# Optimization experiments

Measured on AMD Instinct MI355X. Metric: run time of the kernel, lower is better.

The kernel has to match this reference:

```python
import jax, jax.numpy as jnp
import numpy as np

HID = 4096      # hidden_size
H = 32          # num_attention_heads
K = 8           # num_key_value_heads
D = HID // H    # head_dim = 128
G = H // K      # q heads per kv group = 4
INTER = 14336   # intermediate_size
T = 2048        # tokens (prefill)
EPS = 1e-5
THETA = 1000000.0


def setup_inputs() -> dict:
    key = jax.random.key(0)
    ks = jax.random.split(key, 9)
    s = 0.02
    return {
        "hidden_states": jax.random.normal(ks[0], (T, HID), jnp.float32),
        "position_ids": jnp.arange(T, dtype=jnp.int64),
        "wqkv": jax.random.normal(ks[1], ((H + 2 * K) * D, HID), jnp.float32) * s,
        "wo": jax.random.normal(ks[2], (HID, HID), jnp.float32) * s,
        "w1": jax.random.normal(ks[3], (INTER, HID), jnp.float32) * s,  # gate
        "w3": jax.random.normal(ks[4], (INTER, HID), jnp.float32) * s,  # up
        "w2": jax.random.normal(ks[5], (HID, INTER), jnp.float32) * s,  # down
        "attn_norm_w": jnp.ones((HID,), jnp.float32),
        "ffn_norm_w": jnp.ones((HID,), jnp.float32),
    }


def _rmsnorm(x, w):
    var = jnp.mean(jnp.square(x), axis=-1, keepdims=True)
    return x * jax.lax.rsqrt(var + EPS) * w


def _rope(x, cos, sin):
    # non-interleaved (half-split) rotation; x: [T, h, D], cos/sin: [T, 1, D//2]
    x1, x2 = x[..., : D // 2], x[..., D // 2 :]
    return jnp.concatenate([x1 * cos - x2 * sin, x2 * cos + x1 * sin], axis=-1)


def _attention(x, position_ids, wqkv, wo):
    t = x.shape[0]
    qkv = x @ wqkv.T  # [T, (H+2K)*D]
    q = qkv[:, : H * D].reshape(t, H, D)
    k = qkv[:, H * D : (H + K) * D].reshape(t, K, D)
    v = qkv[:, (H + K) * D :].reshape(t, K, D)

    inv_freq = 1.0 / (THETA ** (jnp.arange(0, D, 2, dtype=jnp.float32) / D))
    freqs = position_ids.astype(jnp.float32)[:, None] * inv_freq  # [T, D//2]
    cos = jnp.cos(freqs)[:, None, :]
    sin = jnp.sin(freqs)[:, None, :]
    q = _rope(q, cos, sin)
    k = _rope(k, cos, sin)

    # grouped-query attention: [T, K, G, D] queries vs [T, K, D] keys
    qg = q.reshape(t, K, G, D)
    scale = 1.0 / jnp.sqrt(jnp.float32(D))
    scores = jnp.einsum("tkgd,skd->kgts", qg, k) * scale  # [K, G, T, T]
    causal = jnp.tril(jnp.ones((t, t), dtype=bool))
    scores = jnp.where(causal, scores, jnp.finfo(scores.dtype).min)
    probs = jax.nn.softmax(scores, axis=-1)
    out = jnp.einsum("kgts,skd->tkgd", probs, v).reshape(t, H * D)
    return out @ wo.T


def _mlp(x, w1, w3, w2):
    return (jax.nn.silu(x @ w1.T) * (x @ w3.T)) @ w2.T


def reference(hidden_states, position_ids, wqkv, wo, w1, w3, w2, attn_norm_w, ffn_norm_w):
    h = hidden_states + _attention(_rmsnorm(hidden_states, attn_norm_w), position_ids, wqkv, wo)
    return h + _mlp(_rmsnorm(h, ffn_norm_w), w1, w3, w2)
```

## Files before the change

### kernel.cpp

```cpp
#include <hip/hip_runtime.h>
#include <stdint.h>

#define T_SEQ 2048
#define HIDN  4096
#define NH    32
#define NKV   8
#define DH    128
#define INTER 14336
#define QKV_N 6144
#define EPSR  1e-5f
#define SCALE 0.08838834764831845f
#define KVB   64

typedef __bf16 bf16x8 __attribute__((ext_vector_type(8)));
typedef float  f32x4  __attribute__((ext_vector_type(4)));

__device__ __forceinline__ f32x4 mfma16(bf16x8 a, bf16x8 b, f32x4 c) {
  return __builtin_amdgcn_mfma_f32_16x16x32_bf16(a, b, c, 0, 0, 0);
}

__device__ __forceinline__ void glds16(const void* g, void* l) {
  __builtin_amdgcn_global_load_lds(
      (__attribute__((address_space(1))) void*)g,
      (__attribute__((address_space(3))) void*)l,
      16, 0, 0);
}

__global__ __launch_bounds__(256) void cvt_bf16_kernel(
    const float* __restrict__ src, __bf16* __restrict__ dst, long n) {
  long stride = (long)gridDim.x * 256 * 8;
  for (long i = ((long)blockIdx.x * 256 + threadIdx.x) * 8; i < n; i += stride) {
    float4 a = *(const float4*)(src + i);
    float4 b = *(const float4*)(src + i + 4);
    bf16x8 o;
    o[0]=(__bf16)a.x; o[1]=(__bf16)a.y; o[2]=(__bf16)a.z; o[3]=(__bf16)a.w;
    o[4]=(__bf16)b.x; o[5]=(__bf16)b.y; o[6]=(__bf16)b.z; o[7]=(__bf16)b.w;
    *(bf16x8*)(dst + i) = o;
  }
}

__global__ __launch_bounds__(256) void rmsnorm_kernel(
    const float* __restrict__ x, const float* __restrict__ w,
    __bf16* __restrict__ y) {
  const int row = blockIdx.x, tid = threadIdx.x;
  const float* xr = x + (size_t)row * HIDN + tid * 16;
  float4 v0 = ((const float4*)xr)[0];
  float4 v1 = ((const float4*)xr)[1];
  float4 v2 = ((const float4*)xr)[2];
  float4 v3 = ((const float4*)xr)[3];
  float ss = v0.x*v0.x + v0.y*v0.y + v0.z*v0.z + v0.w*v0.w
           + v1.x*v1.x + v1.y*v1.y + v1.z*v1.z + v1.w*v1.w
           + v2.x*v2.x + v2.y*v2.y + v2.z*v2.z + v2.w*v2.w
           + v3.x*v3.x + v3.y*v3.y + v3.z*v3.z + v3.w*v3.w;
  #pragma unroll
  for (int off = 32; off >= 1; off >>= 1) ss += __shfl_xor(ss, off, 64);
  __shared__ float red[4];
  if ((tid & 63) == 0) red[tid >> 6] = ss;
  __syncthreads();
  float rn = rsqrtf((red[0] + red[1] + red[2] + red[3]) * (1.0f / HIDN) + EPSR);
  const float* wr = w + tid * 16;
  float4 w0 = ((const float4*)wr)[0];
  float4 w1v = ((const float4*)wr)[1];
  float4 w2v = ((const float4*)wr)[2];
  float4 w3v = ((const float4*)wr)[3];
  bf16x8 o0, o1;
  o0[0]=(__bf16)(v0.x*rn*w0.x);  o0[1]=(__bf16)(v0.y*rn*w0.y);
  o0[2]=(__bf16)(v0.z*rn*w0.z);  o0[3]=(__bf16)(v0.w*rn*w0.w);
  o0[4]=(__bf16)(v1.x*rn*w1v.x); o0[5]=(__bf16)(v1.y*rn*w1v.y);
  o0[6]=(__bf16)(v1.z*rn*w1v.z); o0[7]=(__bf16)(v1.w*rn*w1v.w);
  o1[0]=(__bf16)(v2.x*rn*w2v.x); o1[1]=(__bf16)(v2.y*rn*w2v.y);
  o1[2]=(__bf16)(v2.z*rn*w2v.z); o1[3]=(__bf16)(v2.w*rn*w2v.w);
  o1[4]=(__bf16)(v3.x*rn*w3v.x); o1[5]=(__bf16)(v3.y*rn*w3v.y);
  o1[6]=(__bf16)(v3.z*rn*w3v.z); o1[7]=(__bf16)(v3.w*rn*w3v.w);
  __bf16* yo = y + (size_t)row * HIDN + tid * 16;
  *(bf16x8*)(yo)     = o0;
  *(bf16x8*)(yo + 8) = o1;
}

template<int EPI>
__global__ __launch_bounds__(512, 2) void gemm256_kernel(
    const __bf16* __restrict__ A, const __bf16* __restrict__ B,
    void* __restrict__ Cout, int M, int N, int Kfull, int KZ) {
  extern __shared__ __align__(16) char smem[];
  const int tid = threadIdx.x;
  const int lane = tid & 63;
  const int wv = tid >> 6;
  const int wm = wv >> 2;
  const int wn = wv & 3;
  const int lr = lane & 15, ql = lane >> 4;

  const int gx = gridDim.x, gy = gridDim.y;
  const int nwg = gx * gy;
  const int orig = blockIdx.y * gx + blockIdx.x;
  const int cpx = nwg >> 3;
  const int swz = (orig & 7) * cpx + (orig >> 3);
  const int by = swz % gy, bx = swz / gy;
  const int m0 = by * 256, n0 = bx * 256;
  const int kbase = blockIdx.z * KZ;
  const int NT = KZ >> 6;

  const int u0 = tid, u1 = tid + 512;
  const int r0 = u0 >> 2, r1 = u1 >> 2;
  const int p0 = (u0 & 3) ^ ((r0 >> 1) & 3);
  const int p1 = (u1 & 3) ^ ((r1 >> 1) & 3);
  const char* aR0 = (const char*)(A + (size_t)(m0 + r0) * Kfull + kbase) + p0 * 16;
  const char* aR1 = (const char*)(A + (size_t)(m0 + r1) * Kfull + kbase) + p1 * 16;
  const char* bR0 = (const char*)(B + (size_t)(n0 + r0) * Kfull + kbase) + p0 * 16;
  const char* bR1 = (const char*)(B + (size_t)(n0 + r1) * Kfull + kbase) + p1 * 16;
  const int d0 = u0 * 16, d1 = u1 * 16;

  const int sA = ql ^ ((lr >> 1) & 3);
  int aoff[8], boff[4];
  #pragma unroll
  for (int mt = 0; mt < 8; mt++) aoff[mt] = (wm * 128 + mt * 16 + lr) * 64 + sA * 16;
  #pragma unroll
  for (int nt = 0; nt < 4; nt++) boff[nt] = (wn * 64 + nt * 16 + lr) * 64 + sA * 16;

#define STAGE_A(t, kh, b) do {                                         \
    const size_t _o = (size_t)(t) * 128 + (kh) * 64;                   \
    glds16(aR0 + _o, smem + (b) * 65536 + (kh) * 16384 + d0);          \
    glds16(aR1 + _o, smem + (b) * 65536 + (kh) * 16384 + d1);          \
  } while (0)
#define STAGE_B(t, kh, b) do {                                         \
    const size_t _o = (size_t)(t) * 128 + (kh) * 64;                   \
    glds16(bR0 + _o, smem + (b) * 65536 + 32768 + (kh) * 16384 + d0);  \
    glds16(bR1 + _o, smem + (b) * 65536 + 32768 + (kh) * 16384 + d1);  \
  } while (0)
#define LDA4(dst, mb, b, ks) do {                                      \
    const char* _p = smem + (b) * 65536 + (ks) * 16384;                \
    dst[0] = *(const bf16x8*)(_p + aoff[(mb) + 0]);                    \
    dst[1] = *(const bf16x8*)(_p + aoff[(mb) + 1]);                    \
    dst[2] = *(const bf16x8*)(_p + aoff[(mb) + 2]);                    \
    dst[3] = *(const bf16x8*)(_p + aoff[(mb) + 3]);                    \
  } while (0)
#define LDB4(b, ks) do {                                               \
    const char* _p = smem + (b) * 65536 + 32768 + (ks) * 16384;        \
    bfr[0] = *(const bf16x8*)(_p + boff[0]);                           \
    bfr[1] = *(const bf16x8*)(_p + boff[1]);                           \
    bfr[2] = *(const bf16x8*)(_p + boff[2]);                           \
    bfr[3] = *(const bf16x8*)(_p + boff[3]);                           \
  } while (0)
#define VMW8() asm volatile("s_waitcnt vmcnt(8)" ::: "memory")
#define BAR()  __builtin_amdgcn_s_barrier()
#define WAITK() do { asm volatile("s_waitcnt lgkmcnt(0)" ::: "memory"); \
    __builtin_amdgcn_sched_barrier(0); } while (0)
#define MFMA16(mb, AF) do {                                            \
    __builtin_amdgcn_s_setprio(1);                                     \
    _Pragma("unroll") for (int _m = 0; _m < 4; _m++)                   \
      _Pragma("unroll") for (int _n = 0; _n < 4; _n++)                 \
        acc[(mb) + _m][_n] = mfma16(AF[_m], bfr[_n], acc[(mb) + _m][_n]); \
    __builtin_amdgcn_s_setprio(0);                                     \
  } while (0)

  f32x4 acc[8][4] = {};
  bf16x8 afA[4], afB[4], bfr[4];

  STAGE_A(0, 0, 0); STAGE_B(0, 0, 0);
  STAGE_A(0, 1, 0); STAGE_B(0, 1, 0);
  STAGE_A(1, 0, 1); STAGE_B(1, 0, 1);
  VMW8();
  BAR();

  const int NI = NT >> 1;
  for (int i = 0; i < NI; ++i) {
    const int t1 = 2 * i + 1;
    const int s2 = (2 * i + 2 < NT) ? 2 * i + 2 : NT - 1;
    const int s3 = (2 * i + 3 < NT) ? 2 * i + 3 : NT - 1;
    LDA4(afA, 0, 0, 0); LDB4(0, 0);
    STAGE_A(t1, 1, 1);
    BAR(); WAITK(); MFMA16(0, afA); BAR();
    LDA4(afB, 4, 0, 0);
    STAGE_B(t1, 1, 1);
    VMW8(); BAR(); WAITK(); MFMA16(4, afB); BAR();
    LDA4(afA, 0, 0, 1); LDB4(0, 1);
    STAGE_A(s2, 0, 0);
    BAR(); WAITK(); MFMA16(0, afA); BAR();
    LDA4(afB, 4, 0, 1);
    STAGE_B(s2, 0, 0);
    VMW8(); BAR(); WAITK(); MFMA16(4, afB); BAR();
    LDA4(afA, 0, 1, 0); LDB4(1, 0);
    STAGE_A(s2, 1, 0);
    BAR(); WAITK(); MFMA16(0, afA); BAR();
    LDA4(afB, 4, 1, 0);
    STAGE_B(s2, 1, 0);
    VMW8(); BAR(); WAITK(); MFMA16(4, afB); BAR();
    LDA4(afA, 0, 1, 1); LDB4(1, 1);
    STAGE_A(s3, 0, 1);
    BAR(); WAITK(); MFMA16(0, afA); BAR();
    LDA4(afB, 4, 1, 1);
    STAGE_B(s3, 0, 1);
    VMW8(); BAR(); WAITK(); MFMA16(4, afB); BAR();
  }
  asm volatile("s_waitcnt vmcnt(0)" ::: "memory");

#undef STAGE_A
#undef STAGE_B
#undef LDA4
#undef LDB4
#undef VMW8
#undef BAR
#undef WAITK
#undef MFMA16

  #pragma unroll
  for (int mt = 0; mt < 8; mt++) {
    #pragma unroll
    for (int r = 0; r < 4; r++) {
      int rr = m0 + wm * 128 + mt * 16 + ql * 4 + r;
      #pragma unroll
      for (int nt = 0; nt < 4; nt++) {
        int cc = n0 + wn * 64 + nt * 16 + lr;
        size_t ix = (size_t)rr * N + cc;
        float val = acc[mt][nt][r];
        if (EPI == 0) ((float*)Cout)[(size_t)blockIdx.z * M * N + ix] = val;
        else          ((__bf16*)Cout)[ix] = (__bf16)val;
      }
    }
  }
}

__global__ __launch_bounds__(256) void add3_kernel(
    const float* __restrict__ p, const float* __restrict__ r,
    float* __restrict__ o, long n) {
  long stride = (long)gridDim.x * 1024;
  for (long i = ((long)blockIdx.x * 256 + threadIdx.x) * 4; i < n; i += stride) {
    float4 a = *(const float4*)(p + i);
    float4 b = *(const float4*)(p + n + i);
    float4 c = *(const float4*)(r + i);
    float4 o4;
    o4.x = a.x + b.x + c.x; o4.y = a.y + b.y + c.y;
    o4.z = a.z + b.z + c.z; o4.w = a.w + b.w + c.w;
    *(float4*)(o + i) = o4;
  }
}

__global__ __launch_bounds__(256) void rope_kernel(
    const __bf16* __restrict__ qkv, __bf16* __restrict__ q_r,
    __bf16* __restrict__ k_r) {
  const int t = blockIdx.x, tid = threadIdx.x;
  __shared__ float cs[64], sn[64];
  if (tid < 64) {
    float inv = exp2f(-(float)tid * (19.931568569324174f / 64.0f));
    float f = (float)t * inv;
    cs[tid] = cosf(f);
    sn[tid] = sinf(f);
  }
  __syncthreads();
  const __bf16* row = qkv + (size_t)t * QKV_N;
  for (int it = tid; it < 40 * 64; it += 256) {
    int hh = it >> 6, i = it & 63;
    float x1 = (float)row[hh * 128 + i];
    float x2 = (float)row[hh * 128 + 64 + i];
    float c = cs[i], s = sn[i];
    float o1 = x1 * c - x2 * s;
    float o2 = x2 * c + x1 * s;
    if (hh < NH) {
      __bf16* qo = q_r + (size_t)t * HIDN + hh * 128;
      qo[i] = (__bf16)o1;
      qo[64 + i] = (__bf16)o2;
    } else {
      __bf16* ko = k_r + (size_t)t * (NKV * DH) + (hh - NH) * 128;
      ko[i] = (__bf16)o1;
      ko[64 + i] = (__bf16)o2;
    }
  }
}

__global__ __launch_bounds__(256) void vtrans_kernel(
    const __bf16* __restrict__ qkv, __bf16* __restrict__ v_t) {
  __shared__ __bf16 tile[64][136];
  const int tid = threadIdx.x;
  const int t0 = blockIdx.x * 64, kh = blockIdx.y;
  #pragma unroll
  for (int i = 0; i < 4; i++) {
    int u = i * 256 + tid;
    int row = u >> 4, c = (u & 15) * 8;
    *(bf16x8*)&tile[row][c] =
        *(const bf16x8*)(qkv + (size_t)(t0 + row) * QKV_N + (NH + NKV) * DH + kh * DH + c);
  }
  __syncthreads();
  const int d = tid & 127, th = (tid >> 7) * 32;
  #pragma unroll
  for (int j = 0; j < 4; j++) {
    int t = th + j * 8;
    bf16x8 o;
    #pragma unroll
    for (int e = 0; e < 8; e++) o[e] = tile[t + e][d];
    *(bf16x8*)(v_t + ((size_t)kh * DH + d) * T_SEQ + t0 + t) = o;
  }
}

__global__ __launch_bounds__(256) void attn_kernel(
    const __bf16* __restrict__ q_r, const __bf16* __restrict__ k_r,
    const __bf16* __restrict__ v_t, __bf16* __restrict__ attn_o) {
  __shared__ __align__(16) __bf16 Ks[KVB * 128];
  __shared__ __align__(16) __bf16 Vs[128 * KVB];
  __shared__ __align__(16) __bf16 Pl[4 * 16 * KVB];

  const int tid = threadIdx.x;
  const int lane = tid & 63, wv = tid >> 6;
  const int lr = lane & 15, g = lane >> 4;
  const int qt = gridDim.x - 1 - blockIdx.x;
  const int h = blockIdx.y;
  const int kh = h >> 2;
  const int q0b = qt * 64;
  const int q0w = q0b + wv * 16;

  bf16x8 qf[4];
  {
    const __bf16* qp = q_r + (size_t)(q0w + lr) * HIDN + h * DH + g * 8;
    #pragma unroll
    for (int kk = 0; kk < 4; kk++) qf[kk] = *(const bf16x8*)(qp + kk * 32);
  }

  f32x4 o[8] = {};
  float mrun[4] = {-1e30f, -1e30f, -1e30f, -1e30f};
  float lrun[4] = {0.f, 0.f, 0.f, 0.f};
  char* PlW = (char*)Pl + wv * 2048;

  for (int kv0 = 0; kv0 < q0b + KVB; kv0 += KVB) {
    __syncthreads();
    #pragma unroll
    for (int i = 0; i < 4; i++) {
      int u = i * 256 + tid;
      int row = u >> 4;
      int cb = ((u & 15) * 16) ^ ((row & 7) << 4);
      glds16((const char*)(k_r + (size_t)(kv0 + row) * (NKV * DH) + kh * DH) + cb,
             (char*)Ks + u * 16);
    }
    #pragma unroll
    for (int i = 0; i < 4; i++) {
      int u = i * 256 + tid;
      int row = u >> 3;
      int cb = ((u & 7) * 16) ^ ((row & 7) << 4);
      glds16((const char*)(v_t + ((size_t)kh * DH + row) * T_SEQ + kv0) + cb,
             (char*)Vs + u * 16);
    }
    __syncthreads();

    if (q0w + 15 >= kv0) {
      f32x4 s[4] = {};
      #pragma unroll
      for (int kk = 0; kk < 4; kk++) {
        #pragma unroll
        for (int jt = 0; jt < 4; jt++) {
          int krow = jt * 16 + lr;
          int cb = (kk * 64 + g * 16) ^ ((krow & 7) << 4);
          bf16x8 kf = *(const bf16x8*)((char*)Ks + krow * 256 + cb);
          s[jt] = mfma16(qf[kk], kf, s[jt]);
        }
      }
      const bool need_mask = (kv0 + KVB - 1) > q0w;
      #pragma unroll
      for (int r = 0; r < 4; r++) {
        int qpos = q0w + g * 4 + r;
        int prow = g * 4 + r;
        float p[4];
        #pragma unroll
        for (int jt = 0; jt < 4; jt++) {
          float v = s[jt][r] * SCALE;
          if (need_mask && (kv0 + jt * 16 + lr > qpos)) v = -1e30f;
          p[jt] = v;
        }
        float mx = fmaxf(fmaxf(p[0], p[1]), fmaxf(p[2], p[3]));
        #pragma unroll
        for (int off = 1; off < 16; off <<= 1) mx = fmaxf(mx, __shfl_xor(mx, off, 64));
        float mn = fmaxf(mrun[r], mx);
        float corr = __expf(mrun[r] - mn);
        mrun[r] = mn;
        float ps = 0.f;
        #pragma unroll
        for (int jt = 0; jt < 4; jt++) {
          p[jt] = __expf(p[jt] - mn);
          ps += p[jt];
          int cbyte = ((jt * 16 + lr) * 2) ^ ((prow & 7) << 4);
          *(__bf16*)(PlW + prow * 128 + cbyte) = (__bf16)p[jt];
        }
        #pragma unroll
        for (int off = 1; off < 16; off <<= 1) ps += __shfl_xor(ps, off, 64);
        lrun[r] = lrun[r] * corr + ps;
        #pragma unroll
        for (int nt = 0; nt < 8; nt++) o[nt][r] *= corr;
      }
      bf16x8 pa[2];
      #pragma unroll
      for (int ks = 0; ks < 2; ks++)
        pa[ks] = *(const bf16x8*)(PlW + lr * 128 + ((g * 16 + ks * 64) ^ ((lr & 7) << 4)));
      #pragma unroll
      for (int nt = 0; nt < 8; nt++) {
        #pragma unroll
        for (int ks = 0; ks < 2; ks++) {
          int vrow = nt * 16 + lr;
          int cb = (ks * 64 + g * 16) ^ ((vrow & 7) << 4);
          bf16x8 vf = *(const bf16x8*)((char*)Vs + vrow * 128 + cb);
          o[nt] = mfma16(pa[ks], vf, o[nt]);
        }
      }
    }
  }

  #pragma unroll
  for (int nt = 0; nt < 8; nt++) {
    #pragma unroll
    for (int r = 0; r < 4; r++) {
      int qrow = q0w + g * 4 + r;
      int d = nt * 16 + lr;
      attn_o[(size_t)qrow * HIDN + h * DH + d] = (__bf16)(o[nt][r] / lrun[r]);
    }
  }
}

__global__ __launch_bounds__(256) void silu_mul_kernel(
    const __bf16* __restrict__ u, const __bf16* __restrict__ v,
    __bf16* __restrict__ g, long n) {
  long stride = (long)gridDim.x * 256 * 8;
  for (long i = ((long)blockIdx.x * 256 + threadIdx.x) * 8; i < n; i += stride) {
    bf16x8 uu = *(const bf16x8*)(u + i);
    bf16x8 vv = *(const bf16x8*)(v + i);
    bf16x8 gg;
    #pragma unroll
    for (int j = 0; j < 8; j++) {
      float x = (float)uu[j];
      float y = (float)vv[j];
      float sl = x / (1.0f + __expf(-x));
      gg[j] = (__bf16)(sl * y);
    }
    *(bf16x8*)(g + i) = gg;
  }
}

extern "C" void kernel_launch(void* const* d_in, const int* in_sizes, int n_in,
                              void* d_out, int out_size, void* d_ws, size_t ws_size,
                              hipStream_t stream) {
  const float* hidden = (const float*)d_in[0];
  const float* wqkv = (const float*)d_in[2];
  const float* wo   = (const float*)d_in[3];
  const float* w1   = (const float*)d_in[4];
  const float* w3   = (const float*)d_in[5];
  const float* w2   = (const float*)d_in[6];
  const float* anw  = (const float*)d_in[7];
  const float* fnw  = (const float*)d_in[8];

  char* ws = (char*)d_ws;
  const size_t SZ_XN   = (size_t)T_SEQ * HIDN * 2;
  const size_t SZ_QKV  = (size_t)T_SEQ * QKV_N * 2;
  const size_t SZ_KR   = (size_t)T_SEQ * NKV * DH * 2;
  const size_t SZ_H    = (size_t)T_SEQ * HIDN * 4;
  const size_t SZ_UV   = (size_t)T_SEQ * INTER * 2;

  const size_t W_QKV = (size_t)QKV_N * HIDN * 2;
  const size_t W_O   = (size_t)HIDN * HIDN * 2;
  const size_t W_I   = (size_t)INTER * HIDN * 2;
  const size_t W_TOTAL = W_QKV + W_O + 3 * W_I;

  char* act = ws + W_TOTAL;

  __bf16* xn1    = (__bf16*)(act);
  __bf16* qkv    = (__bf16*)(act + SZ_XN);
  __bf16* q_r    = (__bf16*)(act + SZ_XN + SZ_QKV);
  __bf16* ubuf   = (__bf16*)(act);
  __bf16* k_r    = (__bf16*)(act + SZ_UV);
  __bf16* attn_o = (__bf16*)(act + SZ_UV + SZ_KR);
  float*  hbuf   = (float*) (act + SZ_UV + SZ_KR + SZ_XN);
  __bf16* v_t    = (__bf16*)(act + SZ_UV + SZ_KR + SZ_XN);
  __bf16* xn2    = (__bf16*)(act + SZ_UV + SZ_KR + SZ_XN + SZ_H);
  __bf16* vbuf   = (__bf16*)(act + SZ_UV + SZ_KR + SZ_XN + SZ_H + SZ_XN);
  __bf16* gbuf   = ubuf;
  float*  pbuf   = (float*)(act + SZ_UV + SZ_KR + SZ_XN + SZ_H);

  __bf16* wqkv_b = (__bf16*)(ws);
  __bf16* wo_b   = (__bf16*)(ws + W_QKV);
  __bf16* w1_b   = (__bf16*)(ws + W_QKV + W_O);
  __bf16* w3_b   = (__bf16*)(ws + W_QKV + W_O + W_I);
  __bf16* w2_b   = (__bf16*)(ws + W_QKV + W_O + 2 * W_I);

  const int LDS_BYTES = 131072;
  hipFuncSetAttribute((const void*)gemm256_kernel<0>,
                      hipFuncAttributeMaxDynamicSharedMemorySize, LDS_BYTES);
  hipFuncSetAttribute((const void*)gemm256_kernel<1>,
                      hipFuncAttributeMaxDynamicSharedMemorySize, LDS_BYTES);

  cvt_bf16_kernel<<<2048, 256, 0, stream>>>(wqkv, wqkv_b, (long)QKV_N * HIDN);
  cvt_bf16_kernel<<<2048, 256, 0, stream>>>(wo,   wo_b,   (long)HIDN * HIDN);
  cvt_bf16_kernel<<<2048, 256, 0, stream>>>(w1,   w1_b,   (long)INTER * HIDN);
  cvt_bf16_kernel<<<2048, 256, 0, stream>>>(w3,   w3_b,   (long)INTER * HIDN);
  cvt_bf16_kernel<<<2048, 256, 0, stream>>>(w2,   w2_b,   (long)HIDN * INTER);

  rmsnorm_kernel<<<T_SEQ, 256, 0, stream>>>(hidden, anw, xn1);
  gemm256_kernel<1><<<dim3(QKV_N / 256, T_SEQ / 256, 1), 512, LDS_BYTES, stream>>>(
      xn1, wqkv_b, qkv, T_SEQ, QKV_N, HIDN, HIDN);
  rope_kernel<<<T_SEQ, 256, 0, stream>>>(qkv, q_r, k_r);
  vtrans_kernel<<<dim3(T_SEQ / 64, NKV), 256, 0, stream>>>(qkv, v_t);
  attn_kernel<<<dim3(T_SEQ / 64, NH), 256, 0, stream>>>(q_r, k_r, v_t, attn_o);
  gemm256_kernel<0><<<dim3(HIDN / 256, T_SEQ / 256, 2), 512, LDS_BYTES, stream>>>(
      attn_o, wo_b, pbuf, T_SEQ, HIDN, HIDN, HIDN / 2);
  add3_kernel<<<2048, 256, 0, stream>>>(pbuf, hidden, hbuf, (long)T_SEQ * HIDN);
  rmsnorm_kernel<<<T_SEQ, 256, 0, stream>>>(hbuf, fnw, xn2);
  gemm256_kernel<1><<<dim3(INTER / 256, T_SEQ / 256, 1), 512, LDS_BYTES, stream>>>(
      xn2, w1_b, ubuf, T_SEQ, INTER, HIDN, HIDN);
  gemm256_kernel<1><<<dim3(INTER / 256, T_SEQ / 256, 1), 512, LDS_BYTES, stream>>>(
      xn2, w3_b, vbuf, T_SEQ, INTER, HIDN, HIDN);
  silu_mul_kernel<<<2048, 256, 0, stream>>>(ubuf, vbuf, gbuf, (long)T_SEQ * INTER);
  gemm256_kernel<0><<<dim3(HIDN / 256, T_SEQ / 256, 2), 512, LDS_BYTES, stream>>>(
      gbuf, w2_b, pbuf, T_SEQ, HIDN, INTER, INTER / 2);
  add3_kernel<<<2048, 256, 0, stream>>>(pbuf, hbuf, (float*)d_out, (long)T_SEQ * HIDN);
}
```

Baseline: 1.326 ms.

## Fuse gate/up GEMMs with SiLU epilogue and fuse residual add with RMSNorm

Interleaves w1 and w3 rows during the bf16 conversion so a single GEMM computes gate and up columns for the same output in one tile, then applies SiLU*mul in the epilogue and writes only the gated bf16 result. This removes the separate silu_mul kernel and the write and re-read of the two intermediate T x INTER buffers. It also fuses the attention split-K reduction and residual add with the second RMSNorm into one kernel, saving a pass over the hidden state. Workspace buffers are remapped to fit the new layout. The cost is a more complex weight-permutation kernel and an epilogue that depends on the exact warp tile layout.

Measured after the change: 1.290 ms. -2.7%, faster.

```diff
diff --git a/kernel.cpp b/kernel.cpp
--- a/kernel.cpp
+++ b/kernel.cpp
@@ -36,6 +36,30 @@
     o[0]=(__bf16)a.x; o[1]=(__bf16)a.y; o[2]=(__bf16)a.z; o[3]=(__bf16)a.w;
     o[4]=(__bf16)b.x; o[5]=(__bf16)b.y; o[6]=(__bf16)b.z; o[7]=(__bf16)b.w;
     *(bf16x8*)(dst + i) = o;
+  }
+}
+
+__global__ __launch_bounds__(256) void cvt_w13_kernel(
+    const float* __restrict__ w1, const float* __restrict__ w3,
+    __bf16* __restrict__ dst) {
+  for (int c = blockIdx.x; c < 2 * INTER; c += gridDim.x) {
+    int tau = c >> 8, j2 = c & 255;
+    int wn = j2 >> 6, j = j2 & 63, nt = j >> 4, k16 = j & 15;
+    const float* src = (nt < 2 ? w1 : w3) +
+        (size_t)(tau * 128 + wn * 32 + (nt & 1) * 16 + k16) * HIDN;
+    __bf16* d = dst + (size_t)c * HIDN;
+    int i = threadIdx.x * 16;
+    float4 a = *(const float4*)(src + i);
+    float4 b = *(const float4*)(src + i + 4);
+    float4 e = *(const float4*)(src + i + 8);
+    float4 f = *(const float4*)(src + i + 12);
+    bf16x8 o0, o1;
+    o0[0]=(__bf16)a.x; o0[1]=(__bf16)a.y; o0[2]=(__bf16)a.z; o0[3]=(__bf16)a.w;
+    o0[4]=(__bf16)b.x; o0[5]=(__bf16)b.y; o0[6]=(__bf16)b.z; o0[7]=(__bf16)b.w;
+    o1[0]=(__bf16)e.x; o1[1]=(__bf16)e.y; o1[2]=(__bf16)e.z; o1[3]=(__bf16)e.w;
+    o1[4]=(__bf16)f.x; o1[5]=(__bf16)f.y; o1[6]=(__bf16)f.z; o1[7]=(__bf16)f.w;
+    *(bf16x8*)(d + i) = o0;
+    *(bf16x8*)(d + i + 8) = o1;
   }
 }
 
@@ -59,28 +83,60 @@
   __syncthreads();
   float rn = rsqrtf((red[0] + red[1] + red[2] + red[3]) * (1.0f / HIDN) + EPSR);
   const float* wr = w + tid * 16;
-  float4 w0 = ((const float4*)wr)[0];
-  float4 w1v = ((const float4*)wr)[1];
-  float4 w2v = ((const float4*)wr)[2];
-  float4 w3v = ((const float4*)wr)[3];
-  bf16x8 o0, o1;
-  o0[0]=(__bf16)(v0.x*rn*w0.x);  o0[1]=(__bf16)(v0.y*rn*w0.y);
-  o0[2]=(__bf16)(v0.z*rn*w0.z);  o0[3]=(__bf16)(v0.w*rn*w0.w);
-  o0[4]=(__bf16)(v1.x*rn*w1v.x); o0[5]=(__bf16)(v1.y*rn*w1v.y);
-  o0[6]=(__bf16)(v1.z*rn*w1v.z); o0[7]=(__bf16)(v1.w*rn*w1v.w);
-  o1[0]=(__bf16)(v2.x*rn*w2v.x); o1[1]=(__bf16)(v2.y*rn*w2v.y);
-  o1[2]=(__bf16)(v2.z*rn*w2v.z); o1[3]=(__bf16)(v2.w*rn*w2v.w);
-  o1[4]=(__bf16)(v3.x*rn*w3v.x); o1[5]=(__bf16)(v3.y*rn*w3v.y);
-  o1[6]=(__bf16)(v3.z*rn*w3v.z); o1[7]=(__bf16)(v3.w*rn*w3v.w);
-  __bf16* yo = y + (size_t)row * HIDN + tid * 16;
-  *(bf16x8*)(yo)     = o0;
-  *(bf16x8*)(yo + 8) = o1;
+  #pragma unroll
+  for (int h = 0; h < 2; h++) {
+    float4 a = ((const float4*)xr)[h*2], b = ((const float4*)xr)[h*2+1];
+    float4 wa = ((const float4*)wr)[h*2], wb = ((const float4*)wr)[h*2+1];
+    bf16x8 o;
+    o[0]=(__bf16)(a.x*rn*wa.x); o[1]=(__bf16)(a.y*rn*wa.y);
+    o[2]=(__bf16)(a.z*rn*wa.z); o[3]=(__bf16)(a.w*rn*wa.w);
+    o[4]=(__bf16)(b.x*rn*wb.x); o[5]=(__bf16)(b.y*rn*wb.y);
+    o[6]=(__bf16)(b.z*rn*wb.z); o[7]=(__bf16)(b.w*rn*wb.w);
+    *(bf16x8*)(y + (size_t)row * HIDN + tid * 16 + h * 8) = o;
+  }
+}
+
+__global__ __launch_bounds__(256) void add3_rms_kernel(
+    const float* __restrict__ p, const float* __restrict__ resid,
+    const float* __restrict__ w, float* __restrict__ hout,
+    __bf16* __restrict__ xn) {
+  const int row = blockIdx.x, tid = threadIdx.x;
+  const size_t base = (size_t)row * HIDN + tid * 16;
+  const size_t half = (size_t)T_SEQ * HIDN;
+  float h[16];
+  float ss = 0.f;
+  #pragma unroll
+  for (int q = 0; q < 4; q++) {
+    float4 a = *(const float4*)(p + base + q * 4);
+    float4 b = *(const float4*)(p + half + base + q * 4);
+    float4 c = *(const float4*)(resid + base + q * 4);
+    h[q*4+0] = a.x + b.x + c.x; h[q*4+1] = a.y + b.y + c.y;
+    h[q*4+2] = a.z + b.z + c.z; h[q*4+3] = a.w + b.w + c.w;
+    ss += h[q*4]*h[q*4] + h[q*4+1]*h[q*4+1] + h[q*4+2]*h[q*4+2] + h[q*4+3]*h[q*4+3];
+    *(float4*)(hout + base + q * 4) = *(float4*)&h[q*4];
+  }
+  #pragma unroll
+  for (int off = 32; off >= 1; off >>= 1) ss += __shfl_xor(ss, off, 64);
+  __shared__ float red[4];
+  if ((tid & 63) == 0) red[tid >> 6] = ss;
+  __syncthreads();
+  float rn = rsqrtf((red[0] + red[1] + red[2] + red[3]) * (1.0f / HIDN) + EPSR);
+  #pragma unroll
+  for (int hb = 0; hb < 2; hb++) {
+    bf16x8 o;
+    #pragma unroll
+    for (int e = 0; e < 8; e++) {
+      float wv = w[tid * 16 + hb * 8 + e];
+      o[e] = (__bf16)(h[hb*8+e] * rn * wv);
+    }
+    *(bf16x8*)(xn + base + hb * 8) = o;
+  }
 }
 
 template<int EPI>
 __global__ __launch_bounds__(512, 2) void gemm256_kernel(
     const __bf16* __restrict__ A, const __bf16* __restrict__ B,
-    void* __restrict__ Cout, int M, int N, int Kfull, int KZ) {
+    void* __restrict__ Cout, int M, int N, int Kfull, int KZ, int Nout) {
   extern __shared__ __align__(16) char smem[];
   const int tid = threadIdx.x;
   const int lane = tid & 63;
@@ -207,13 +263,24 @@
     #pragma unroll
     for (int r = 0; r < 4; r++) {
       int rr = m0 + wm * 128 + mt * 16 + ql * 4 + r;
-      #pragma unroll
-      for (int nt = 0; nt < 4; nt++) {
-        int cc = n0 + wn * 64 + nt * 16 + lr;
-        size_t ix = (size_t)rr * N + cc;
-        float val = acc[mt][nt][r];
-        if (EPI == 0) ((float*)Cout)[(size_t)blockIdx.z * M * N + ix] = val;
-        else          ((__bf16*)Cout)[ix] = (__bf16)val;
+      if (EPI == 2) {
+        #pragma unroll
+        for (int nt = 0; nt < 2; nt++) {
+          float u = acc[mt][nt][r];
+          float v = acc[mt][nt + 2][r];
+          float g = u / (1.0f + __expf(-u)) * v;
+          int cc = (n0 >> 1) + wn * 32 + nt * 16 + lr;
+          ((__bf16*)Cout)[(size_t)rr * Nout + cc] = (__bf16)g;
+        }
+      } else {
+        #pragma unroll
+        for (int nt = 0; nt < 4; nt++) {
+          int cc = n0 + wn * 64 + nt * 16 + lr;
+          size_t ix = (size_t)rr * N + cc;
+          float val = acc[mt][nt][r];
+          if (EPI == 0) ((float*)Cout)[(size_t)blockIdx.z * M * N + ix] = val;
+          else          ((__bf16*)Cout)[ix] = (__bf16)val;
+        }
       }
     }
   }
@@ -410,25 +477,6 @@
   }
 }
 
-__global__ __launch_bounds__(256) void silu_mul_kernel(
-    const __bf16* __restrict__ u, const __bf16* __restrict__ v,
-    __bf16* __restrict__ g, long n) {
-  long stride = (long)gridDim.x * 256 * 8;
-  for (long i = ((long)blockIdx.x * 256 + threadIdx.x) * 8; i < n; i += stride) {
-    bf16x8 uu = *(const bf16x8*)(u + i);
-    bf16x8 vv = *(const bf16x8*)(v + i);
-    bf16x8 gg;
-    #pragma unroll
-    for (int j = 0; j < 8; j++) {
-      float x = (float)uu[j];
-      float y = (float)vv[j];
-      float sl = x / (1.0f + __expf(-x));
-      gg[j] = (__bf16)(sl * y);
-    }
-    *(bf16x8*)(g + i) = gg;
-  }
-}
-
 extern "C" void kernel_launch(void* const* d_in, const int* in_sizes, int n_in,
                               void* d_out, int out_size, void* d_ws, size_t ws_size,
                               hipStream_t stream) {
@@ -458,20 +506,17 @@
   __bf16* xn1    = (__bf16*)(act);
   __bf16* qkv    = (__bf16*)(act + SZ_XN);
   __bf16* q_r    = (__bf16*)(act + SZ_XN + SZ_QKV);
-  __bf16* ubuf   = (__bf16*)(act);
+  __bf16* gbuf   = (__bf16*)(act);
   __bf16* k_r    = (__bf16*)(act + SZ_UV);
   __bf16* attn_o = (__bf16*)(act + SZ_UV + SZ_KR);
   float*  hbuf   = (float*) (act + SZ_UV + SZ_KR + SZ_XN);
   __bf16* v_t    = (__bf16*)(act + SZ_UV + SZ_KR + SZ_XN);
   __bf16* xn2    = (__bf16*)(act + SZ_UV + SZ_KR + SZ_XN + SZ_H);
-  __bf16* vbuf   = (__bf16*)(act + SZ_UV + SZ_KR + SZ_XN + SZ_H + SZ_XN);
-  __bf16* gbuf   = ubuf;
-  float*  pbuf   = (float*)(act + SZ_UV + SZ_KR + SZ_XN + SZ_H);
+  float*  pbuf   = (float*)(act + SZ_UV + SZ_KR + SZ_XN + SZ_H + SZ_XN);
 
   __bf16* wqkv_b = (__bf16*)(ws);
   __bf16* wo_b   = (__bf16*)(ws + W_QKV);
-  __bf16* w1_b   = (__bf16*)(ws + W_QKV + W_O);
-  __bf16* w3_b   = (__bf16*)(ws + W_QKV + W_O + W_I);
+  __bf16* w13_b  = (__bf16*)(ws + W_QKV + W_O);
   __bf16* w2_b   = (__bf16*)(ws + W_QKV + W_O + 2 * W_I);
 
   const int LDS_BYTES = 131072;
@@ -479,29 +524,26 @@
                       hipFuncAttributeMaxDynamicSharedMemorySize, LDS_BYTES);
   hipFuncSetAttribute((const void*)gemm256_kernel<1>,
                       hipFuncAttributeMaxDynamicSharedMemorySize, LDS_BYTES);
+  hipFuncSetAttribute((const void*)gemm256_kernel<2>,
+                      hipFuncAttributeMaxDynamicSharedMemorySize, LDS_BYTES);
 
   cvt_bf16_kernel<<<2048, 256, 0, stream>>>(wqkv, wqkv_b, (long)QKV_N * HIDN);
   cvt_bf16_kernel<<<2048, 256, 0, stream>>>(wo,   wo_b,   (long)HIDN * HIDN);
-  cvt_bf16_kernel<<<2048, 256, 0, stream>>>(w1,   w1_b,   (long)INTER * HIDN);
-  cvt_bf16_kernel<<<2048, 256, 0, stream>>>(w3,   w3_b,   (long)INTER * HIDN);
+  cvt_w13_kernel<<<2048, 256, 0, stream>>>(w1, w3, w13_b);
   cvt_bf16_kernel<<<2048, 256, 0, stream>>>(w2,   w2_b,   (long)HIDN * INTER);
 
   rmsnorm_kernel<<<T_SEQ, 256, 0, stream>>>(hidden, anw, xn1);
   gemm256_kernel<1><<<dim3(QKV_N / 256, T_SEQ / 256, 1), 512, LDS_BYTES, stream>>>(
-      xn1, wqkv_b, qkv, T_SEQ, QKV_N, HIDN, HIDN);
+      xn1, wqkv_b, qkv, T_SEQ, QKV_N, HIDN, HIDN, QKV_N);
   rope_kernel<<<T_SEQ, 256, 0, stream>>>(qkv, q_r, k_r);
   vtrans_kernel<<<dim3(T_SEQ / 64, NKV), 256, 0, stream>>>(qkv, v_t);
   attn_kernel<<<dim3(T_SEQ / 64, NH), 256, 0, stream>>>(q_r, k_r, v_t, attn_o);
   gemm256_kernel<0><<<dim3(HIDN / 256, T_SEQ / 256, 2), 512, LDS_BYTES, stream>>>(
-      attn_o, wo_b, pbuf, T_SEQ, HIDN, HIDN, HIDN / 2);
-  add3_kernel<<<2048, 256, 0, stream>>>(pbuf, hidden, hbuf, (long)T_SEQ * HIDN);
-  rmsnorm_kernel<<<T_SEQ, 256, 0, stream>>>(hbuf, fnw, xn2);
-  gemm256_kernel<1><<<dim3(INTER / 256, T_SEQ / 256, 1), 512, LDS_BYTES, stream>>>(
-      xn2, w1_b, ubuf, T_SEQ, INTER, HIDN, HIDN);
-  gemm256_kernel<1><<<dim3(INTER / 256, T_SEQ / 256, 1), 512, LDS_BYTES, stream>>>(
-      xn2, w3_b, vbuf, T_SEQ, INTER, HIDN, HIDN);
-  silu_mul_kernel<<<2048, 256, 0, stream>>>(ubuf, vbuf, gbuf, (long)T_SEQ * INTER);
+      attn_o, wo_b, pbuf, T_SEQ, HIDN, HIDN, HIDN / 2, HIDN);
+  add3_rms_kernel<<<T_SEQ, 256, 0, stream>>>(pbuf, hidden, fnw, hbuf, xn2);
+  gemm256_kernel<2><<<dim3(2 * INTER / 256, T_SEQ / 256, 1), 512, LDS_BYTES, stream>>>(
+      xn2, w13_b, gbuf, T_SEQ, 2 * INTER, HIDN, HIDN, INTER);
   gemm256_kernel<0><<<dim3(HIDN / 256, T_SEQ / 256, 2), 512, LDS_BYTES, stream>>>(
-      gbuf, w2_b, pbuf, T_SEQ, HIDN, INTER, INTER / 2);
+      gbuf, w2_b, pbuf, T_SEQ, HIDN, INTER, INTER / 2, HIDN);
   add3_kernel<<<2048, 256, 0, stream>>>(pbuf, hbuf, (float*)d_out, (long)T_SEQ * HIDN);
 }
```
